# Kernel tuning notes

Measured on AMD Instinct MI355X. Metric: run time of the kernel, lower is better.

## Reference

```python
import jax, jax.numpy as jnp
import numpy as np

N_NODES = 50000
N_EDGES = 800000
C = 128
EDGE_DIM = 8
N_LAYERS = 3


def setup_inputs() -> dict:
    key = jax.random.key(0)
    ks = jax.random.split(key, 8)
    x = jax.random.normal(ks[0], (N_NODES, C), dtype=jnp.float32)
    edge_index = jax.random.randint(ks[1], (2, N_EDGES), 0, N_NODES, dtype=jnp.int64)
    edge_attr = jax.random.uniform(ks[2], (N_EDGES, EDGE_DIM), dtype=jnp.float32)
    # stacked per-layer params (all layers are 128->128 HydroConv)
    lin_w = jax.random.normal(ks[3], (N_LAYERS, C, C), dtype=jnp.float32) / np.sqrt(C)
    lin_b = jnp.zeros((N_LAYERS, C), dtype=jnp.float32)
    emlp_w = jax.random.normal(ks[4], (N_LAYERS, EDGE_DIM, 1), dtype=jnp.float32) / np.sqrt(EDGE_DIM)
    emlp_b = jnp.zeros((N_LAYERS, 1), dtype=jnp.float32)
    return {"x": x, "edge_index": edge_index, "edge_attr": edge_attr,
            "lin_w": lin_w, "lin_b": lin_b, "emlp_w": emlp_w, "emlp_b": emlp_b}


def _hydro_conv(x, src, dst, edge_attr, lw, lb, ew, eb):
    # edge weight: softplus(edge_attr @ ew + eb) -> [E, 1]
    weight = jax.nn.softplus(edge_attr @ ew + eb)
    # message: weight * (x_j - x_i), x_j = source, x_i = target
    msg = weight * (x[src] - x[dst])                  # [E, C]
    agg = jax.ops.segment_sum(msg, dst, num_segments=N_NODES)  # scatter-add at target
    return agg @ lw + lb                              # node linear


def reference(x, edge_index, edge_attr, lin_w, lin_b, emlp_w, emlp_b):
    src, dst = edge_index[0], edge_index[1]
    for i in range(N_LAYERS):
        residual = x
        x = _hydro_conv(x, src, dst, edge_attr, lin_w[i], lin_b[i], emlp_w[i], emlp_b[i])
        if i < N_LAYERS - 1:
            x = jax.nn.relu(x)
            x = x + residual  # residual=True, dropout=0
    return x
```

## Files before the change

### kernel.cpp

```cpp
#include <hip/hip_runtime.h>

#define NN 50000
#define NE 800000
#define CC 128
#define NL 3

typedef short bf16x8 __attribute__((ext_vector_type(8)));
typedef float f32x4 __attribute__((ext_vector_type(4)));
union U16 { uint4 u; bf16x8 v; };

__device__ __forceinline__ float b2f(unsigned short u) {
  return __uint_as_float(((unsigned int)u) << 16);
}
__device__ __forceinline__ unsigned short f2b(float f) {
  unsigned int x = __float_as_uint(f);
  x += 0x7fffu + ((x >> 16) & 1u);
  return (unsigned short)(x >> 16);
}

__global__ void k_flags(const unsigned short* __restrict__ x,
                        const int* __restrict__ ei, int* __restrict__ flags) {
  __shared__ int cnt, any;
  if (threadIdx.x == 0) { cnt = 0; any = 0; }
  __syncthreads();
  if (threadIdx.x < 128) {
    unsigned short u = x[2 * threadIdx.x];
    int ex = (u >> 7) & 0xFF;
    if (ex >= 0x70 && ex <= 0x8F) atomicAdd(&cnt, 1);
  }
  if (ei[2 * threadIdx.x + 1] != 0) atomicOr(&any, 1);
  __syncthreads();
  if (threadIdx.x == 0) {
    flags[0] = (cnt >= 64) ? 1 : 0;
    flags[1] = (any == 0) ? 1 : 0;
  }
}

__device__ __forceinline__ int eidx(const int* ei, int row, int e, int f64) {
  return f64 ? ei[2 * ((size_t)row * NE + e)] : ei[(size_t)row * NE + e];
}

__global__ __launch_bounds__(256) void k_cvt_x(const void* __restrict__ xin,
                                               unsigned short* __restrict__ xb,
                                               const int* __restrict__ flags) {
  if (flags[0]) return;
  int i = blockIdx.x * 256 + threadIdx.x;
  const float4 a = ((const float4*)xin)[2 * i];
  const float4 b = ((const float4*)xin)[2 * i + 1];
  uint4 o;
  o.x = (unsigned)f2b(a.x) | ((unsigned)f2b(a.y) << 16);
  o.y = (unsigned)f2b(a.z) | ((unsigned)f2b(a.w) << 16);
  o.z = (unsigned)f2b(b.x) | ((unsigned)f2b(b.y) << 16);
  o.w = (unsigned)f2b(b.z) | ((unsigned)f2b(b.w) << 16);
  ((uint4*)xb)[i] = o;
}

__global__ __launch_bounds__(256) void k_cvt_par(const void* lw, const void* lb,
                                                 const void* emw, const void* emb,
                                                 unsigned short* __restrict__ wt,
                                                 float* lbf, float* emwf, float* embf,
                                                 const int* __restrict__ flags) {
  int i = blockIdx.x * 256 + threadIdx.x;
  const int bf = flags[0];
  if (i < NL * CC * CC) {
    unsigned short v = bf ? ((const unsigned short*)lw)[i]
                          : f2b(((const float*)lw)[i]);
    const int l = i >> 14, r = i & 16383, k = r >> 7, n = r & 127;
    wt[l * 16384 + n * 128 + k] = v;
  }
  if (i < NL * CC)
    lbf[i] = bf ? b2f(((const unsigned short*)lb)[i]) : ((const float*)lb)[i];
  if (i < NL * 8)
    emwf[i] = bf ? b2f(((const unsigned short*)emw)[i]) : ((const float*)emw)[i];
  if (i < NL)
    embf[i] = bf ? b2f(((const unsigned short*)emb)[i]) : ((const float*)emb)[i];
}

#define HT 8
#define HIST_BLKS ((NE + HT * 256 - 1) / (HT * 256))
__global__ __launch_bounds__(256) void k_hist(const int* __restrict__ ei,
                                              int* __restrict__ deg,
                                              unsigned short* __restrict__ rank,
                                              const int* __restrict__ flags) {
  const int f64 = flags[1];
  const int nt = gridDim.x * 256;
  const int t = blockIdx.x * 256 + threadIdx.x;
  int d[HT], r[HT];
#pragma unroll
  for (int k = 0; k < HT; ++k) {
    const int e = t + k * nt;
    d[k] = (e < NE) ? eidx(ei, 1, e, f64) : -1;
  }
#pragma unroll
  for (int k = 0; k < HT; ++k)
    if (d[k] >= 0) r[k] = atomicAdd(&deg[d[k]], 1);
#pragma unroll
  for (int k = 0; k < HT; ++k) {
    const int e = t + k * nt;
    if (e < NE) rank[e] = (unsigned short)r[k];
  }
}

#define NI4 (NN / 4)
#define SCAN_BLKS ((NI4 + 255) / 256)
__global__ __launch_bounds__(256) void k_scan1(const int* __restrict__ deg,
                                               int* __restrict__ offs,
                                               int* __restrict__ bsum) {
  __shared__ int ls[256];
  const int t = threadIdx.x;
  const int g = blockIdx.x * 256 + t;
  int4 d = make_int4(0, 0, 0, 0);
  if (g < NI4) d = ((const int4*)deg)[g];
  const int s = d.x + d.y + d.z + d.w;
  ls[t] = s;
  __syncthreads();
#pragma unroll
  for (int off = 1; off < 256; off <<= 1) {
    int tmp = (t >= off) ? ls[t - off] : 0;
    __syncthreads();
    ls[t] += tmp;
    __syncthreads();
  }
  const int excl = ls[t] - s;
  if (g < NI4) {
    int4 o;
    o.x = excl; o.y = o.x + d.x; o.z = o.y + d.y; o.w = o.z + d.z;
    ((int4*)offs)[g] = o;
  }
  if (t == 255) bsum[blockIdx.x] = ls[255];
}

__global__ void k_scan2(const int* __restrict__ bsum, int* __restrict__ bbase,
                        int* __restrict__ offs) {
  if (threadIdx.x == 0) {
    int run = 0;
    for (int b = 0; b < SCAN_BLKS; ++b) { bbase[b] = run; run += bsum[b]; }
    offs[NN] = run;
  }
}

__global__ __launch_bounds__(256) void k_scan3(int* __restrict__ offs,
                                               const int* __restrict__ bbase) {
  const int g = blockIdx.x * 256 + threadIdx.x;
  if (g >= NI4) return;
  const int base = bbase[blockIdx.x];
  int4 o = ((int4*)offs)[g];
  o.x += base; o.y += base; o.z += base; o.w += base;
  ((int4*)offs)[g] = o;
}

__global__ __launch_bounds__(256) void k_fill(const int* __restrict__ ei,
                                              const void* __restrict__ ea,
                                              const float* __restrict__ emwf,
                                              const float* __restrict__ embf,
                                              const int* __restrict__ offs,
                                              const unsigned short* __restrict__ rank,
                                              uint4* __restrict__ esrt,
                                              const int* __restrict__ flags) {
  int e = blockIdx.x * 256 + threadIdx.x;
  if (e >= NE) return;
  float a[8];
  if (flags[0]) {
    const uint4 v = ((const uint4*)ea)[e];
    unsigned int p[4] = {v.x, v.y, v.z, v.w};
#pragma unroll
    for (int q = 0; q < 4; ++q) {
      a[2 * q]     = __uint_as_float(p[q] << 16);
      a[2 * q + 1] = __uint_as_float(p[q] & 0xffff0000u);
    }
  } else {
    const float4 v0 = ((const float4*)ea)[2 * e];
    const float4 v1 = ((const float4*)ea)[2 * e + 1];
    a[0] = v0.x; a[1] = v0.y; a[2] = v0.z; a[3] = v0.w;
    a[4] = v1.x; a[5] = v1.y; a[6] = v1.z; a[7] = v1.w;
  }
  float w[NL];
#pragma unroll
  for (int l = 0; l < NL; ++l) {
    float z = embf[l];
#pragma unroll
    for (int k = 0; k < 8; ++k) z += a[k] * emwf[l * 8 + k];
    w[l] = (z > 20.f) ? z : log1pf(expf(z));
  }
  const int f64 = flags[1];
  const int d = eidx(ei, 1, e, f64);
  const int s = eidx(ei, 0, e, f64);
  const int pos = offs[d] + (int)rank[e];
  esrt[pos] = make_uint4((unsigned)s, __float_as_uint(w[0]),
                         __float_as_uint(w[1]), __float_as_uint(w[2]));
}

template<int LAYER>
__device__ __forceinline__ unsigned wcomp(const uint4& p) {
  return LAYER == 0 ? p.y : (LAYER == 1 ? p.z : p.w);
}

template<int LAYER>
__global__ __launch_bounds__(256) void k_gather(const int* __restrict__ offs,
                                                const uint4* __restrict__ esrt,
                                                const unsigned short* xb_,
                                                const unsigned short* alt, int sel,
                                                unsigned short* __restrict__ agg,
                                                const int* __restrict__ flags) {
  const unsigned short* xb = (sel && flags[0]) ? alt : xb_;
  const int node =
      __builtin_amdgcn_readfirstlane(blockIdx.x * 4 + (threadIdx.x >> 6));
  const int l = threadIdx.x & 63;
  const int g = l >> 4;
  const int ch = (l & 15) * 8;
  const int j0 = offs[node];
  const int j1 = offs[node + 1];

  const uint4 xi = *(const uint4*)&xb[(size_t)node * CC + ch];

  float ax[8];
#pragma unroll
  for (int i = 0; i < 8; ++i) ax[i] = 0.f;
  float sw = 0.f;

  for (int jc = j0; jc < j1; jc += 64) {
    const int cnt = j1 - jc;
    const int kk = (l < cnt) ? l : (cnt - 1);
    const uint4 rec = esrt[jc + kk];
    const int srcl = (int)rec.x;
    const int wl = (int)wcomp<LAYER>(rec);
    const int nsb = (cnt + 15) >> 4;
    for (int b2 = 0; b2 < nsb; ++b2) {
      int srcw[4]; float wv[4];
#pragma unroll
      for (int b = 0; b < 4; ++b) {
        const int k = b2 * 16 + b * 4 + g;
        srcw[b] = __shfl(srcl, k);
        const float w = __uint_as_float((unsigned)__shfl(wl, k));
        wv[b] = (k < cnt) ? w : 0.f;
      }
      uint4 v[4];
#pragma unroll
      for (int b = 0; b < 4; ++b)
        v[b] = *(const uint4*)&xb[(size_t)(unsigned)srcw[b] * CC + ch];
#pragma unroll
      for (int b = 0; b < 4; ++b) {
        const float w = wv[b];
        const unsigned pv0 = v[b].x, pv1 = v[b].y, pv2 = v[b].z, pv3 = v[b].w;
        ax[0] += w * __uint_as_float(pv0 << 16);
        ax[1] += w * __uint_as_float(pv0 & 0xffff0000u);
        ax[2] += w * __uint_as_float(pv1 << 16);
        ax[3] += w * __uint_as_float(pv1 & 0xffff0000u);
        ax[4] += w * __uint_as_float(pv2 << 16);
        ax[5] += w * __uint_as_float(pv2 & 0xffff0000u);
        ax[6] += w * __uint_as_float(pv3 << 16);
        ax[7] += w * __uint_as_float(pv3 & 0xffff0000u);
        sw += w;
      }
    }
  }

#pragma unroll
  for (int i = 0; i < 8; ++i) {
    ax[i] += __shfl_xor(ax[i], 16);
    ax[i] += __shfl_xor(ax[i], 32);
  }
  sw += __shfl_xor(sw, 16);
  sw += __shfl_xor(sw, 32);

  if (l < 16) {
    float r[8];
    r[0] = ax[0] - sw * __uint_as_float(xi.x << 16);
    r[1] = ax[1] - sw * __uint_as_float(xi.x & 0xffff0000u);
    r[2] = ax[2] - sw * __uint_as_float(xi.y << 16);
    r[3] = ax[3] - sw * __uint_as_float(xi.y & 0xffff0000u);
    r[4] = ax[4] - sw * __uint_as_float(xi.z << 16);
    r[5] = ax[5] - sw * __uint_as_float(xi.z & 0xffff0000u);
    r[6] = ax[6] - sw * __uint_as_float(xi.w << 16);
    r[7] = ax[7] - sw * __uint_as_float(xi.w & 0xffff0000u);
    uint4 o;
    o.x = (unsigned)f2b(r[0]) | ((unsigned)f2b(r[1]) << 16);
    o.y = (unsigned)f2b(r[2]) | ((unsigned)f2b(r[3]) << 16);
    o.z = (unsigned)f2b(r[4]) | ((unsigned)f2b(r[5]) << 16);
    o.w = (unsigned)f2b(r[6]) | ((unsigned)f2b(r[7]) << 16);
    *(uint4*)&agg[(size_t)node * CC + ch] = o;
  }
}

#define LPAD 136
__global__ __launch_bounds__(256) void k_gemm(unsigned short* agg,
                                              const unsigned short* xc_,
                                              const unsigned short* alt,
                                              int sel,
                                              const unsigned short* __restrict__ wt,
                                              const float* __restrict__ lbf,
                                              int layer, void* outp, int last,
                                              const int* __restrict__ flags) {
  const unsigned short* xc = (sel && flags[0]) ? alt : xc_;
  __shared__ unsigned short shA[64 * LPAD];
  __shared__ unsigned short shB[128 * LPAD];
  const int rb = blockIdx.x * 64;
  const unsigned short* wtl = wt + (size_t)layer * CC * CC;

  for (int u = threadIdx.x; u < 1024; u += 256) {
    const int row = u >> 4, q = u & 15;
    uint4 v = make_uint4(0, 0, 0, 0);
    if (rb + row < NN) v = *(const uint4*)&agg[(size_t)(rb + row) * CC + q * 8];
    *(uint4*)&shA[row * LPAD + q * 8] = v;
  }
  for (int u = threadIdx.x; u < 2048; u += 256) {
    const int row = u >> 4, q = u & 15;
    *(uint4*)&shB[row * LPAD + q * 8] = *(const uint4*)&wtl[row * 128 + q * 8];
  }
  __syncthreads();

  const int w = threadIdx.x >> 6;
  const int l = threadIdx.x & 63;
  const int lr = l & 15;
  const int lk = (l >> 4) * 8;

  U16 afr[4];
#pragma unroll
  for (int kk = 0; kk < 4; ++kk)
    afr[kk].u = *(const uint4*)&shA[(w * 16 + lr) * LPAD + kk * 32 + lk];

  const float* lbp = lbf + layer * CC;
  f32x4 acc[8];
#pragma unroll
  for (int t = 0; t < 8; ++t) {
    acc[t] = (f32x4){0.f, 0.f, 0.f, 0.f};
#pragma unroll
    for (int kk = 0; kk < 4; ++kk) {
      U16 bfr;
      bfr.u = *(const uint4*)&shB[(t * 16 + lr) * LPAD + kk * 32 + lk];
      acc[t] = __builtin_amdgcn_mfma_f32_16x16x32_bf16(afr[kk].v, bfr.v, acc[t], 0, 0, 0);
    }
  }

#pragma unroll
  for (int t = 0; t < 8; ++t) {
    const float bv = lbp[t * 16 + lr];
#pragma unroll
    for (int r = 0; r < 4; ++r) {
      const int tr = (l >> 4) * 4 + r;
      shA[(w * 16 + tr) * LPAD + t * 16 + lr] = f2b(acc[t][r] + bv);
    }
  }
  const int isbf = flags[0];
#pragma unroll
  for (int i = 0; i < 8; ++i) {
    const int idx = i * 64 + l;
    const int row = idx >> 5, cg = idx & 31;
    const int gr = rb + w * 16 + row;
    if (gr >= NN) continue;
    const uint2 yv = *(const uint2*)&shA[(w * 16 + row) * LPAD + cg * 4];
    float y0 = __uint_as_float(yv.x << 16);
    float y1 = __uint_as_float(yv.x & 0xffff0000u);
    float y2 = __uint_as_float(yv.y << 16);
    float y3 = __uint_as_float(yv.y & 0xffff0000u);
    const size_t off = (size_t)gr * CC + cg * 4;
    if (!last) {
      const uint2 rv = *(const uint2*)&xc[off];
      y0 = fmaxf(y0, 0.f) + __uint_as_float(rv.x << 16);
      y1 = fmaxf(y1, 0.f) + __uint_as_float(rv.x & 0xffff0000u);
      y2 = fmaxf(y2, 0.f) + __uint_as_float(rv.y << 16);
      y3 = fmaxf(y3, 0.f) + __uint_as_float(rv.y & 0xffff0000u);
      *(uint2*)&agg[off] = make_uint2((unsigned)f2b(y0) | ((unsigned)f2b(y1) << 16),
                                      (unsigned)f2b(y2) | ((unsigned)f2b(y3) << 16));
    } else if (isbf) {
      *(uint2*)&((unsigned short*)outp)[off] = yv;
    } else {
      *(float4*)&((float*)outp)[off] = make_float4(y0, y1, y2, y3);
    }
  }
}

extern "C" void kernel_launch(void* const* d_in, const int* in_sizes, int n_in,
                              void* d_out, int out_size, void* d_ws, size_t ws_size,
                              hipStream_t stream) {
  const unsigned short* x0 = (const unsigned short*)d_in[0];
  const int* ei = (const int*)d_in[1];

  const size_t nbuf = (size_t)NN * CC;
  unsigned short* xb0 = (unsigned short*)d_ws;
  unsigned short* xb1 = xb0 + nbuf;
  unsigned short* wt = xb1 + nbuf;
  uint4* esrt = (uint4*)(wt + (size_t)NL * CC * CC);
  int* deg = (int*)(esrt + NE);
  int* offs = deg + NN;
  unsigned short* rank = (unsigned short*)(offs + NN + 4);
  int* bsum = (int*)(rank + NE);
  int* bbase = bsum + 64;
  float* lbf = (float*)(bbase + 64);
  float* emwf = lbf + (size_t)NL * CC;
  float* embf = emwf + NL * 8;
  int* flags = (int*)(embf + NL);
  const size_t need = (size_t)((char*)(flags + 2) - (char*)d_ws);
  if (ws_size < need) {
    hipMemsetAsync(d_out, 0, (size_t)out_size * 2, stream);
    return;
  }

  k_flags<<<1, 256, 0, stream>>>(x0, ei, flags);
  k_cvt_x<<<(NN * CC / 8) / 256, 256, 0, stream>>>(d_in[0], xb0, flags);
  k_cvt_par<<<(NL * CC * CC + 255) / 256, 256, 0, stream>>>(
      d_in[3], d_in[4], d_in[5], d_in[6], wt, lbf, emwf, embf, flags);

  hipMemsetAsync(deg, 0, NN * sizeof(int), stream);
  k_hist<<<HIST_BLKS, 256, 0, stream>>>(ei, deg, rank, flags);
  k_scan1<<<SCAN_BLKS, 256, 0, stream>>>(deg, offs, bsum);
  k_scan2<<<1, 64, 0, stream>>>(bsum, bbase, offs);
  k_scan3<<<SCAN_BLKS, 256, 0, stream>>>(offs, bbase);
  k_fill<<<(NE + 255) / 256, 256, 0, stream>>>(ei, d_in[2], emwf, embf,
                                               offs, rank, esrt, flags);

  unsigned short* xc = xb0;
  unsigned short* ag = xb1;
  for (int layer = 0; layer < NL; ++layer) {
    const int sel = (layer == 0) ? 1 : 0;
    if (layer == 0)
      k_gather<0><<<NN / 4, 256, 0, stream>>>(offs, esrt, xc, x0, sel, ag, flags);
    else if (layer == 1)
      k_gather<1><<<NN / 4, 256, 0, stream>>>(offs, esrt, xc, x0, sel, ag, flags);
    else
      k_gather<2><<<NN / 4, 256, 0, stream>>>(offs, esrt, xc, x0, sel, ag, flags);
    k_gemm<<<(NN + 63) / 64, 256, 0, stream>>>(ag, xc, x0, sel, wt, lbf, layer,
                                               d_out, layer == NL - 1 ? 1 : 0, flags);
    unsigned short* t = xc; xc = ag; ag = t;
  }
}
```

Measured before the change: 308.5 us.

## Fuse gather aggregation and node GEMM into one per-layer kernel

Merges the per-node gather/scatter aggregation and the 128x128 node linear into a single 512-thread kernel. Each block aggregates 64 nodes directly into shared memory, then runs the MFMA GEMM with bias, relu and residual from LDS. This removes the bf16 round-trip of the aggregate through global memory and one kernel launch per layer. In exchange there are far fewer, larger blocks (782 vs 12500 gather blocks) with a larger LDS footprint, which may reduce occupancy and latency hiding for the irregular gathers.

```diff
diff --git a/kernel.cpp b/kernel.cpp
--- a/kernel.cpp
+++ b/kernel.cpp
@@ -190,182 +190,188 @@
                          __float_as_uint(w[1]), __float_as_uint(w[2]));
 }
 
+#define LPAD 136
 template<int LAYER>
 __device__ __forceinline__ unsigned wcomp(const uint4& p) {
   return LAYER == 0 ? p.y : (LAYER == 1 ? p.z : p.w);
 }
 
 template<int LAYER>
-__global__ __launch_bounds__(256) void k_gather(const int* __restrict__ offs,
-                                                const uint4* __restrict__ esrt,
-                                                const unsigned short* xb_,
-                                                const unsigned short* alt, int sel,
-                                                unsigned short* __restrict__ agg,
-                                                const int* __restrict__ flags) {
-  const unsigned short* xb = (sel && flags[0]) ? alt : xb_;
-  const int node =
-      __builtin_amdgcn_readfirstlane(blockIdx.x * 4 + (threadIdx.x >> 6));
-  const int l = threadIdx.x & 63;
-  const int g = l >> 4;
-  const int ch = (l & 15) * 8;
-  const int j0 = offs[node];
-  const int j1 = offs[node + 1];
-
-  const uint4 xi = *(const uint4*)&xb[(size_t)node * CC + ch];
-
-  float ax[8];
-#pragma unroll
-  for (int i = 0; i < 8; ++i) ax[i] = 0.f;
-  float sw = 0.f;
-
-  for (int jc = j0; jc < j1; jc += 64) {
-    const int cnt = j1 - jc;
-    const int kk = (l < cnt) ? l : (cnt - 1);
-    const uint4 rec = esrt[jc + kk];
-    const int srcl = (int)rec.x;
-    const int wl = (int)wcomp<LAYER>(rec);
-    const int nsb = (cnt + 15) >> 4;
-    for (int b2 = 0; b2 < nsb; ++b2) {
-      int srcw[4]; float wv[4];
-#pragma unroll
-      for (int b = 0; b < 4; ++b) {
-        const int k = b2 * 16 + b * 4 + g;
-        srcw[b] = __shfl(srcl, k);
-        const float w = __uint_as_float((unsigned)__shfl(wl, k));
-        wv[b] = (k < cnt) ? w : 0.f;
-      }
-      uint4 v[4];
-#pragma unroll
-      for (int b = 0; b < 4; ++b)
-        v[b] = *(const uint4*)&xb[(size_t)(unsigned)srcw[b] * CC + ch];
-#pragma unroll
-      for (int b = 0; b < 4; ++b) {
-        const float w = wv[b];
-        const unsigned pv0 = v[b].x, pv1 = v[b].y, pv2 = v[b].z, pv3 = v[b].w;
-        ax[0] += w * __uint_as_float(pv0 << 16);
-        ax[1] += w * __uint_as_float(pv0 & 0xffff0000u);
-        ax[2] += w * __uint_as_float(pv1 << 16);
-        ax[3] += w * __uint_as_float(pv1 & 0xffff0000u);
-        ax[4] += w * __uint_as_float(pv2 << 16);
-        ax[5] += w * __uint_as_float(pv2 & 0xffff0000u);
-        ax[6] += w * __uint_as_float(pv3 << 16);
-        ax[7] += w * __uint_as_float(pv3 & 0xffff0000u);
-        sw += w;
-      }
-    }
-  }
-
-#pragma unroll
-  for (int i = 0; i < 8; ++i) {
-    ax[i] += __shfl_xor(ax[i], 16);
-    ax[i] += __shfl_xor(ax[i], 32);
-  }
-  sw += __shfl_xor(sw, 16);
-  sw += __shfl_xor(sw, 32);
-
-  if (l < 16) {
-    float r[8];
-    r[0] = ax[0] - sw * __uint_as_float(xi.x << 16);
-    r[1] = ax[1] - sw * __uint_as_float(xi.x & 0xffff0000u);
-    r[2] = ax[2] - sw * __uint_as_float(xi.y << 16);
-    r[3] = ax[3] - sw * __uint_as_float(xi.y & 0xffff0000u);
-    r[4] = ax[4] - sw * __uint_as_float(xi.z << 16);
-    r[5] = ax[5] - sw * __uint_as_float(xi.z & 0xffff0000u);
-    r[6] = ax[6] - sw * __uint_as_float(xi.w << 16);
-    r[7] = ax[7] - sw * __uint_as_float(xi.w & 0xffff0000u);
-    uint4 o;
-    o.x = (unsigned)f2b(r[0]) | ((unsigned)f2b(r[1]) << 16);
-    o.y = (unsigned)f2b(r[2]) | ((unsigned)f2b(r[3]) << 16);
-    o.z = (unsigned)f2b(r[4]) | ((unsigned)f2b(r[5]) << 16);
-    o.w = (unsigned)f2b(r[6]) | ((unsigned)f2b(r[7]) << 16);
-    *(uint4*)&agg[(size_t)node * CC + ch] = o;
-  }
-}
-
-#define LPAD 136
-__global__ __launch_bounds__(256) void k_gemm(unsigned short* agg,
-                                              const unsigned short* xc_,
-                                              const unsigned short* alt,
-                                              int sel,
-                                              const unsigned short* __restrict__ wt,
-                                              const float* __restrict__ lbf,
-                                              int layer, void* outp, int last,
-                                              const int* __restrict__ flags) {
-  const unsigned short* xc = (sel && flags[0]) ? alt : xc_;
+__global__ __launch_bounds__(512) void k_layer(const int* __restrict__ offs,
+                                               const uint4* __restrict__ esrt,
+                                               const unsigned short* xc_,
+                                               const unsigned short* alt, int sel,
+                                               const unsigned short* __restrict__ wt,
+                                               const float* __restrict__ lbf,
+                                               void* outp, int last,
+                                               const int* __restrict__ flags,
+                                               unsigned short* __restrict__ xout) {
+  const unsigned short* xb = (sel && flags[0]) ? alt : xc_;
   __shared__ unsigned short shA[64 * LPAD];
   __shared__ unsigned short shB[128 * LPAD];
+  const int tid = threadIdx.x;
   const int rb = blockIdx.x * 64;
-  const unsigned short* wtl = wt + (size_t)layer * CC * CC;
-
-  for (int u = threadIdx.x; u < 1024; u += 256) {
-    const int row = u >> 4, q = u & 15;
-    uint4 v = make_uint4(0, 0, 0, 0);
-    if (rb + row < NN) v = *(const uint4*)&agg[(size_t)(rb + row) * CC + q * 8];
-    *(uint4*)&shA[row * LPAD + q * 8] = v;
-  }
-  for (int u = threadIdx.x; u < 2048; u += 256) {
+  const unsigned short* wtl = wt + (size_t)LAYER * CC * CC;
+
+  for (int u = tid; u < 2048; u += 512) {
     const int row = u >> 4, q = u & 15;
     *(uint4*)&shB[row * LPAD + q * 8] = *(const uint4*)&wtl[row * 128 + q * 8];
   }
-  __syncthreads();
-
-  const int w = threadIdx.x >> 6;
-  const int l = threadIdx.x & 63;
+
+  const int wid = tid >> 6;
+  const int l = tid & 63;
+  const int g = l >> 4;
+  const int chlane = l & 15;
+  const int ch = chlane * 8;
+
+  for (int i = 0; i < 8; ++i) {
+    const int nl = wid * 8 + i;
+    const int node = __builtin_amdgcn_readfirstlane(rb + nl);
+    if (node >= NN) {
+      if (l < 16) *(uint4*)&shA[nl * LPAD + ch] = make_uint4(0, 0, 0, 0);
+      continue;
+    }
+    const int j0 = offs[node];
+    const int j1 = offs[node + 1];
+    const uint4 xi = *(const uint4*)&xb[(size_t)node * CC + ch];
+    float ax[8];
+#pragma unroll
+    for (int q = 0; q < 8; ++q) ax[q] = 0.f;
+    float sw = 0.f;
+
+    for (int jc = j0; jc < j1; jc += 64) {
+      const int cnt = j1 - jc;
+      const int kk = (l < cnt) ? l : (cnt - 1);
+      const uint4 rec = esrt[jc + kk];
+      const int srcl = (int)rec.x;
+      const int wl = (int)wcomp<LAYER>(rec);
+      const int cc2 = (cnt > 64) ? 64 : cnt;
+      const int nsb = (cc2 + 15) >> 4;
+      for (int b2 = 0; b2 < nsb; ++b2) {
+        int srcw[4]; float wv[4];
+#pragma unroll
+        for (int b = 0; b < 4; ++b) {
+          const int k = b2 * 16 + b * 4 + g;
+          srcw[b] = __shfl(srcl, k);
+          const float w = __uint_as_float((unsigned)__shfl(wl, k));
+          wv[b] = (k < cnt) ? w : 0.f;
+        }
+        uint4 v[4];
+#pragma unroll
+        for (int b = 0; b < 4; ++b)
+          v[b] = *(const uint4*)&xb[(size_t)(unsigned)srcw[b] * CC + ch];
+#pragma unroll
+        for (int b = 0; b < 4; ++b) {
+          const float w = wv[b];
+          const unsigned pv0 = v[b].x, pv1 = v[b].y, pv2 = v[b].z, pv3 = v[b].w;
+          ax[0] += w * __uint_as_float(pv0 << 16);
+          ax[1] += w * __uint_as_float(pv0 & 0xffff0000u);
+          ax[2] += w * __uint_as_float(pv1 << 16);
+          ax[3] += w * __uint_as_float(pv1 & 0xffff0000u);
+          ax[4] += w * __uint_as_float(pv2 << 16);
+          ax[5] += w * __uint_as_float(pv2 & 0xffff0000u);
+          ax[6] += w * __uint_as_float(pv3 << 16);
+          ax[7] += w * __uint_as_float(pv3 & 0xffff0000u);
+          sw += w;
+        }
+      }
+    }
+
+#pragma unroll
+    for (int q = 0; q < 8; ++q) {
+      ax[q] += __shfl_xor(ax[q], 16);
+      ax[q] += __shfl_xor(ax[q], 32);
+    }
+    sw += __shfl_xor(sw, 16);
+    sw += __shfl_xor(sw, 32);
+
+    if (l < 16) {
+      float r[8];
+      r[0] = ax[0] - sw * __uint_as_float(xi.x << 16);
+      r[1] = ax[1] - sw * __uint_as_float(xi.x & 0xffff0000u);
+      r[2] = ax[2] - sw * __uint_as_float(xi.y << 16);
+      r[3] = ax[3] - sw * __uint_as_float(xi.y & 0xffff0000u);
+      r[4] = ax[4] - sw * __uint_as_float(xi.z << 16);
+      r[5] = ax[5] - sw * __uint_as_float(xi.z & 0xffff0000u);
+      r[6] = ax[6] - sw * __uint_as_float(xi.w << 16);
+      r[7] = ax[7] - sw * __uint_as_float(xi.w & 0xffff0000u);
+      uint4 o;
+      o.x = (unsigned)f2b(r[0]) | ((unsigned)f2b(r[1]) << 16);
+      o.y = (unsigned)f2b(r[2]) | ((unsigned)f2b(r[3]) << 16);
+      o.z = (unsigned)f2b(r[4]) | ((unsigned)f2b(r[5]) << 16);
+      o.w = (unsigned)f2b(r[6]) | ((unsigned)f2b(r[7]) << 16);
+      *(uint4*)&shA[nl * LPAD + ch] = o;
+    }
+  }
+  __syncthreads();
+
+  const int rw = wid >> 1;
+  const int cb = (wid & 1) * 4;
   const int lr = l & 15;
   const int lk = (l >> 4) * 8;
 
   U16 afr[4];
 #pragma unroll
   for (int kk = 0; kk < 4; ++kk)
-    afr[kk].u = *(const uint4*)&shA[(w * 16 + lr) * LPAD + kk * 32 + lk];
-
-  const float* lbp = lbf + layer * CC;
-  f32x4 acc[8];
-#pragma unroll
-  for (int t = 0; t < 8; ++t) {
+    afr[kk].u = *(const uint4*)&shA[(rw * 16 + lr) * LPAD + kk * 32 + lk];
+  __syncthreads();
+
+  const float* lbp = lbf + LAYER * CC;
+  f32x4 acc[4];
+#pragma unroll
+  for (int t = 0; t < 4; ++t) {
     acc[t] = (f32x4){0.f, 0.f, 0.f, 0.f};
 #pragma unroll
     for (int kk = 0; kk < 4; ++kk) {
       U16 bfr;
-      bfr.u = *(const uint4*)&shB[(t * 16 + lr) * LPAD + kk * 32 + lk];
+      bfr.u = *(const uint4*)&shB[((cb + t) * 16 + lr) * LPAD + kk * 32 + lk];
       acc[t] = __builtin_amdgcn_mfma_f32_16x16x32_bf16(afr[kk].v, bfr.v, acc[t], 0, 0, 0);
     }
   }
 
 #pragma unroll
-  for (int t = 0; t < 8; ++t) {
-    const float bv = lbp[t * 16 + lr];
+  for (int t = 0; t < 4; ++t) {
+    const float bv = lbp[(cb + t) * 16 + lr];
 #pragma unroll
     for (int r = 0; r < 4; ++r) {
       const int tr = (l >> 4) * 4 + r;
-      shA[(w * 16 + tr) * LPAD + t * 16 + lr] = f2b(acc[t][r] + bv);
-    }
-  }
+      shA[(rw * 16 + tr) * LPAD + (cb + t) * 16 + lr] = f2b(acc[t][r] + bv);
+    }
+  }
+  __syncthreads();
+
   const int isbf = flags[0];
-#pragma unroll
-  for (int i = 0; i < 8; ++i) {
-    const int idx = i * 64 + l;
-    const int row = idx >> 5, cg = idx & 31;
-    const int gr = rb + w * 16 + row;
+  for (int u = tid; u < 1024; u += 512) {
+    const int row = u >> 4, q = u & 15;
+    const int gr = rb + row;
     if (gr >= NN) continue;
-    const uint2 yv = *(const uint2*)&shA[(w * 16 + row) * LPAD + cg * 4];
-    float y0 = __uint_as_float(yv.x << 16);
-    float y1 = __uint_as_float(yv.x & 0xffff0000u);
-    float y2 = __uint_as_float(yv.y << 16);
-    float y3 = __uint_as_float(yv.y & 0xffff0000u);
-    const size_t off = (size_t)gr * CC + cg * 4;
+    const uint4 yv = *(const uint4*)&shA[row * LPAD + q * 8];
+    float y0 = __uint_as_float(yv.x << 16), y1 = __uint_as_float(yv.x & 0xffff0000u);
+    float y2 = __uint_as_float(yv.y << 16), y3 = __uint_as_float(yv.y & 0xffff0000u);
+    float y4 = __uint_as_float(yv.z << 16), y5 = __uint_as_float(yv.z & 0xffff0000u);
+    float y6 = __uint_as_float(yv.w << 16), y7 = __uint_as_float(yv.w & 0xffff0000u);
+    const size_t off = (size_t)gr * CC + q * 8;
     if (!last) {
-      const uint2 rv = *(const uint2*)&xc[off];
+      const uint4 rv = *(const uint4*)&xb[off];
       y0 = fmaxf(y0, 0.f) + __uint_as_float(rv.x << 16);
       y1 = fmaxf(y1, 0.f) + __uint_as_float(rv.x & 0xffff0000u);
       y2 = fmaxf(y2, 0.f) + __uint_as_float(rv.y << 16);
       y3 = fmaxf(y3, 0.f) + __uint_as_float(rv.y & 0xffff0000u);
-      *(uint2*)&agg[off] = make_uint2((unsigned)f2b(y0) | ((unsigned)f2b(y1) << 16),
-                                      (unsigned)f2b(y2) | ((unsigned)f2b(y3) << 16));
+      y4 = fmaxf(y4, 0.f) + __uint_as_float(rv.z << 16);
+      y5 = fmaxf(y5, 0.f) + __uint_as_float(rv.z & 0xffff0000u);
+      y6 = fmaxf(y6, 0.f) + __uint_as_float(rv.w << 16);
+      y7 = fmaxf(y7, 0.f) + __uint_as_float(rv.w & 0xffff0000u);
+      uint4 o;
+      o.x = (unsigned)f2b(y0) | ((unsigned)f2b(y1) << 16);
+      o.y = (unsigned)f2b(y2) | ((unsigned)f2b(y3) << 16);
+      o.z = (unsigned)f2b(y4) | ((unsigned)f2b(y5) << 16);
+      o.w = (unsigned)f2b(y6) | ((unsigned)f2b(y7) << 16);
+      *(uint4*)&xout[off] = o;
     } else if (isbf) {
-      *(uint2*)&((unsigned short*)outp)[off] = yv;
+      *(uint4*)&((unsigned short*)outp)[off] = yv;
     } else {
       *(float4*)&((float*)outp)[off] = make_float4(y0, y1, y2, y3);
+      *(float4*)&((float*)outp)[off + 4] = make_float4(y4, y5, y6, y7);
     }
   }
 }
@@ -409,18 +415,21 @@
   k_fill<<<(NE + 255) / 256, 256, 0, stream>>>(ei, d_in[2], emwf, embf,
                                                offs, rank, esrt, flags);
 
+  const int LBLKS = (NN + 63) / 64;
   unsigned short* xc = xb0;
-  unsigned short* ag = xb1;
+  unsigned short* xo = xb1;
   for (int layer = 0; layer < NL; ++layer) {
     const int sel = (layer == 0) ? 1 : 0;
+    const int last = (layer == NL - 1) ? 1 : 0;
     if (layer == 0)
-      k_gather<0><<<NN / 4, 256, 0, stream>>>(offs, esrt, xc, x0, sel, ag, flags);
+      k_layer<0><<<LBLKS, 512, 0, stream>>>(offs, esrt, xc, x0, sel, wt, lbf,
+                                            d_out, last, flags, xo);
     else if (layer == 1)
-      k_gather<1><<<NN / 4, 256, 0, stream>>>(offs, esrt, xc, x0, sel, ag, flags);
+      k_layer<1><<<LBLKS, 512, 0, stream>>>(offs, esrt, xc, x0, sel, wt, lbf,
+                                            d_out, last, flags, xo);
     else
-      k_gather<2><<<NN / 4, 256, 0, stream>>>(offs, esrt, xc, x0, sel, ag, flags);
-    k_gemm<<<(NN + 63) / 64, 256, 0, stream>>>(ag, xc, x0, sel, wt, lbf, layer,
-                                               d_out, layer == NL - 1 ? 1 : 0, flags);
-    unsigned short* t = xc; xc = ag; ag = t;
-  }
-}
+      k_layer<2><<<LBLKS, 512, 0, stream>>>(offs, esrt, xc, x0, sel, wt, lbf,
+                                            d_out, last, flags, xo);
+    unsigned short* t = xc; xc = xo; xo = t;
+  }
+}
```

Result: no change. 309.4 us (+0.3%).
